# Kernel optimization log

Hardware: AMD Instinct MI355X
Metric: run time of the kernel (lower is better)

The kernel has to match this reference:

```python
import jax, jax.numpy as jnp
import numpy as np

B, P, L = 32, 16, 512
VOCAB, D = 50000, 256  # embed_dim == hidden_dim (required for attn_type='dot')
SCALE, PAGE_SCALE = 10.0, 10.0


def sparsemax(z):
    # z: [..., K]; sort-based sparsemax (Martins & Astudillo 2016)
    K = z.shape[-1]
    zs = jnp.sort(z, axis=-1)[..., ::-1]            # descending
    k = jnp.arange(1, K + 1, dtype=z.dtype)
    cs = jnp.cumsum(zs, axis=-1)
    support = 1.0 + k * zs > cs                     # [..., K] bool
    kmax = jnp.sum(support, axis=-1, keepdims=True) # support size (>=1)
    cs_k = jnp.take_along_axis(cs, kmax.astype(jnp.int32) - 1, axis=-1)
    tau = (cs_k - 1.0) / kmax.astype(z.dtype)
    return jnp.maximum(z - tau, 0.0)


def setup_inputs() -> dict:
    key = jax.random.key(0)
    k1, k2, k3, k4, k5, k6, k7 = jax.random.split(key, 7)
    seq_ids = jax.random.randint(k1, (B, P, L), 0, VOCAB)
    num_pages = jax.random.randint(k2, (B,), 1, P + 1)        # 1..P valid pages
    seq_lengths = jax.random.randint(k3, (B, P), 1, L + 1)    # 1..L valid tokens
    emb_table = jax.random.uniform(k4, (VOCAB, D), jnp.float32, -0.1, 0.1)
    V = jax.random.normal(k5, (D, 1), jnp.float32)
    W = jax.random.normal(k6, (D, 1), jnp.float32)
    dec_w = jax.random.normal(k7, (1, D), jnp.float32) * 0.05  # decoder, no bias
    return {"seq_ids": seq_ids, "num_pages": num_pages, "seq_lengths": seq_lengths,
            "emb_table": emb_table, "V": V, "W": W, "dec_w": dec_w}


def reference(seq_ids, num_pages, seq_lengths, emb_table, V, W, dec_w):
    # Embedding lookup (dropout is identity in eval mode)
    hidden_vecs = emb_table[seq_ids]                         # [B,P,L,D]
    # Word-level scores (attn_type='dot': inter_out = hidden_vecs)
    scores = jnp.einsum('bpld,do->bpl', hidden_vecs, V) / SCALE  # [B,P,L]
    # Ragged word mask: original double loop only masks pages j < num_pages[i]
    pos = jnp.arange(L)[None, None, :]                       # [1,1,L]
    page_idx = jnp.arange(P)[None, :, None]                  # [1,P,1]
    word_mask = (pos >= seq_lengths[:, :, None]) & (page_idx < num_pages[:, None, None])
    scores = jnp.where(word_mask, -999.0, scores)
    attn = jax.nn.softmax(scores, axis=-1)[:, :, None, :]    # [B,P,1,L]
    webpage_vec = jnp.einsum('bpl,bpld->bpd', attn[:, :, 0, :], hidden_vecs)  # [B,P,D]
    # Page-level scores + sparsemax over pages
    page_scores = jnp.einsum('bpd,do->bp', webpage_vec, W) / PAGE_SCALE
    page_mask = jnp.arange(P)[None, :] >= num_pages[:, None]
    page_scores = jnp.where(page_mask, -9999.0, page_scores)
    page_attn = sparsemax(page_scores)[:, None, :]           # [B,1,P]
    final_vec = jnp.einsum('bp,bpd->bd', page_attn[:, 0, :], webpage_vec)  # [B,D]
    senti_scores = final_vec @ dec_w.T                       # [B,1]
    probs = jax.nn.sigmoid(senti_scores)
    return (probs, senti_scores, attn, page_attn, final_vec, page_scores, webpage_vec)
```

## Files before the change

kernel.cpp:

```cpp
#include <hip/hip_runtime.h>
#include <math.h>

constexpr int Bn = 32, Pn = 16, Ln = 512, Dn = 256, VOC = 50000;
constexpr float QSCALE = 1270.0f, QINV = 1.0f / 1270.0f;

__global__ __launch_bounds__(256) void k_embdot(const float* __restrict__ emb,
                                               const float* __restrict__ V,
                                               const float* __restrict__ W,
                                               float2* __restrict__ eVW,
                                               unsigned char* __restrict__ bt)
{
    int row  = blockIdx.x * 4 + (threadIdx.x >> 6);
    if (row >= VOC) return;
    int lane = threadIdx.x & 63;
    float4 r  = ((const float4*)(emb + (size_t)row * Dn))[lane];
    float4 v  = ((const float4*)V)[lane];
    float4 w  = ((const float4*)W)[lane];

    uint b0 = (uint)((int)rintf(r.x * QSCALE) + 128);
    uint b1 = (uint)((int)rintf(r.y * QSCALE) + 128);
    uint b2 = (uint)((int)rintf(r.z * QSCALE) + 128);
    uint b3 = (uint)((int)rintf(r.w * QSCALE) + 128);
    ((uint*)(bt + (size_t)row * Dn))[lane] = b0 | (b1 << 8) | (b2 << 16) | (b3 << 24);

    float dv = r.x*v.x + r.y*v.y + r.z*v.z + r.w*v.w;
    float dw = r.x*w.x + r.y*w.y + r.z*w.z + r.w*w.w;
#pragma unroll
    for (int o = 32; o; o >>= 1) { dv += __shfl_xor(dv, o); dw += __shfl_xor(dw, o); }
    if (lane == 0) eVW[row] = make_float2(dv / 10.0f, dw / 10.0f);
}

__global__ __launch_bounds__(512) void k_page(const int* __restrict__ seq_ids,
                                              const int* __restrict__ num_pages,
                                              const int* __restrict__ seq_lengths,
                                              const unsigned char* __restrict__ bt,
                                              const float2* __restrict__ eVW,
                                              float* __restrict__ attn_out,
                                              float* __restrict__ pscore_out,
                                              float* __restrict__ web_out)
{
    int bp = blockIdx.x;
    int b  = bp >> 4, p = bp & 15;
    int tid = threadIdx.x, lane = tid & 63, wv = tid >> 6;

    __shared__ int   ids[Ln];
    __shared__ float sc[Ln];
    __shared__ float redm[8], reds[8], redp[8];
    __shared__ float part[32][Dn];

    const int* sid = seq_ids + (size_t)bp * Ln;
    int  slen = seq_lengths[bp];
    bool vp   = (p < num_pages[b]);
    int  Lv   = vp ? slen : Ln;

    int id = sid[tid];
    ids[tid] = id;
    float2 vw = eVW[id];
    float wreg = vw.y;
    sc[tid] = (vp && tid >= slen) ? -999.0f : vw.x;
    __syncthreads();

    float mx = sc[tid];
#pragma unroll
    for (int o = 32; o; o >>= 1) mx = fmaxf(mx, __shfl_xor(mx, o));
    if (lane == 0) redm[wv] = mx;
    __syncthreads();
    mx = redm[0];
#pragma unroll
    for (int w = 1; w < 8; ++w) mx = fmaxf(mx, redm[w]);

    float e = expf(sc[tid] - mx);
    sc[tid] = e;
    float pw = e * wreg;
    float sum = e, ps = pw;
#pragma unroll
    for (int o = 32; o; o >>= 1) { sum += __shfl_xor(sum, o); ps += __shfl_xor(ps, o); }
    if (lane == 0) { reds[wv] = sum; redp[wv] = ps; }
    __syncthreads();
    sum = 0.f; ps = 0.f;
#pragma unroll
    for (int w = 0; w < 8; ++w) { sum += reds[w]; ps += redp[w]; }
    float inv = 1.0f / sum;

    attn_out[(size_t)bp * Ln + tid] = sc[tid] * inv;
    if (tid == 0) pscore_out[bp] = vp ? ps * inv : -9999.0f;

    int s  = 4 * wv + (lane >> 4);
    int cq = lane & 15;
    float a0=0,a1=0,a2=0,a3=0,a4=0,a5=0,a6=0,a7=0,
          a8=0,a9=0,a10=0,a11=0,a12=0,a13=0,a14=0,a15=0;
    float sw = 0.f;
#pragma unroll 4
    for (int l = s; l < Lv; l += 32) {
        float wg = sc[l];
        uint4 q = *(const uint4*)(bt + (size_t)ids[l] * Dn + cq * 16);
        sw  += wg;
        a0  += wg * (float)( q.x        & 0xffu);
        a1  += wg * (float)((q.x >>  8) & 0xffu);
        a2  += wg * (float)((q.x >> 16) & 0xffu);
        a3  += wg * (float)( q.x >> 24         );
        a4  += wg * (float)( q.y        & 0xffu);
        a5  += wg * (float)((q.y >>  8) & 0xffu);
        a6  += wg * (float)((q.y >> 16) & 0xffu);
        a7  += wg * (float)( q.y >> 24         );
        a8  += wg * (float)( q.z        & 0xffu);
        a9  += wg * (float)((q.z >>  8) & 0xffu);
        a10 += wg * (float)((q.z >> 16) & 0xffu);
        a11 += wg * (float)( q.z >> 24         );
        a12 += wg * (float)( q.w        & 0xffu);
        a13 += wg * (float)((q.w >>  8) & 0xffu);
        a14 += wg * (float)((q.w >> 16) & 0xffu);
        a15 += wg * (float)( q.w >> 24         );
    }
    float k = inv * QINV;
    float c = 128.0f * sw;
    float* pr = &part[s][cq * 16];
    ((float4*)pr)[0] = make_float4((a0 -c)*k, (a1 -c)*k, (a2 -c)*k, (a3 -c)*k);
    ((float4*)pr)[1] = make_float4((a4 -c)*k, (a5 -c)*k, (a6 -c)*k, (a7 -c)*k);
    ((float4*)pr)[2] = make_float4((a8 -c)*k, (a9 -c)*k, (a10-c)*k, (a11-c)*k);
    ((float4*)pr)[3] = make_float4((a12-c)*k, (a13-c)*k, (a14-c)*k, (a15-c)*k);
    __syncthreads();

    if (tid < Dn) {
        float acc = 0.f;
#pragma unroll
        for (int w = 0; w < 32; ++w) acc += part[w][tid];
        web_out[(size_t)bp * Dn + tid] = acc;
    }
}

__global__ __launch_bounds__(256) void k_final(const float* __restrict__ dec_w,
                                               const float* __restrict__ pscore,
                                               const float* __restrict__ web,
                                               float* __restrict__ probs,
                                               float* __restrict__ senti,
                                               float* __restrict__ pattn,
                                               float* __restrict__ fvec)
{
    int b = blockIdx.x, tid = threadIdx.x, lane = tid & 63, wv = tid >> 6;
    __shared__ float pa[Pn];
    __shared__ float red[4];

    if (tid == 0) {
        float z[Pn], zs[Pn], csum[Pn];
        for (int i = 0; i < Pn; ++i) { z[i] = pscore[b * Pn + i]; zs[i] = z[i]; }
        for (int i = 1; i < Pn; ++i) {
            float key = zs[i]; int j = i - 1;
            while (j >= 0 && zs[j] < key) { zs[j + 1] = zs[j]; --j; }
            zs[j + 1] = key;
        }
        int kmax = 0; float cs = 0.f;
        for (int k = 0; k < Pn; ++k) {
            cs += zs[k];
            csum[k] = cs;
            if (1.0f + (float)(k + 1) * zs[k] > cs) kmax = k + 1;
        }
        float tau = (csum[kmax - 1] - 1.0f) / (float)kmax;
        for (int i = 0; i < Pn; ++i) pa[i] = fmaxf(z[i] - tau, 0.0f);
    }
    __syncthreads();

    float fv = 0.f;
#pragma unroll
    for (int p = 0; p < Pn; ++p) fv += pa[p] * web[((size_t)b * Pn + p) * Dn + tid];
    fvec[(size_t)b * Dn + tid] = fv;
    if (tid < Pn) pattn[b * Pn + tid] = pa[tid];

    float t = fv * dec_w[tid];
#pragma unroll
    for (int o = 32; o; o >>= 1) t += __shfl_xor(t, o);
    if (lane == 0) red[wv] = t;
    __syncthreads();
    if (tid == 0) {
        float s = red[0] + red[1] + red[2] + red[3];
        senti[b] = s;
        probs[b] = 1.0f / (1.0f + expf(-s));
    }
}

extern "C" void kernel_launch(void* const* d_in, const int* in_sizes, int n_in,
                              void* d_out, int out_size, void* d_ws, size_t ws_size,
                              hipStream_t stream) {
    const int*   seq_ids     = (const int*)d_in[0];
    const int*   num_pages   = (const int*)d_in[1];
    const int*   seq_lengths = (const int*)d_in[2];
    const float* emb         = (const float*)d_in[3];
    const float* V           = (const float*)d_in[4];
    const float* W           = (const float*)d_in[5];
    const float* dec_w       = (const float*)d_in[6];

    float* out    = (float*)d_out;
    float* probs  = out;
    float* senti  = probs + Bn;
    float* attn   = senti + Bn;
    float* pattn  = attn  + (size_t)Bn * Pn * Ln;
    float* fvec   = pattn + Bn * Pn;
    float* pscore = fvec  + (size_t)Bn * Dn;
    float* web    = pscore + Bn * Pn;

    float2* eVW = (float2*)d_ws;
    unsigned char* bt = (unsigned char*)((char*)d_ws + (size_t)VOC * sizeof(float2));

    k_embdot<<<(VOC + 3) / 4, 256, 0, stream>>>(emb, V, W, eVW, bt);
    k_page<<<Bn * Pn, 512, 0, stream>>>(seq_ids, num_pages, seq_lengths,
                                        bt, eVW, attn, pscore, web);
    k_final<<<Bn, 256, 0, stream>>>(dec_w, pscore, web, probs, senti, pattn, fvec);
}
```

Before: 32.17 us.

## Fuse final sparsemax kernel into page kernel via last-block atomic counter

Removes the separate k_final launch. Each page block bumps a per-batch atomic counter, and the last of the 16 page blocks for a batch computes the sparsemax, the final vector, the decoder score and the sigmoid. The counters are zeroed inside k_embdot. The gather loop is also unrolled to process two tokens per iteration at stride 64, which exposes more independent loads. This can over-read tokens past the sequence length, but those carry near-zero softmax weight. The cost is an extra barrier, threadfences and a tail of serial work in one block per batch.

```diff
diff --git a/kernel.cpp b/kernel.cpp
--- a/kernel.cpp
+++ b/kernel.cpp
@@ -8,8 +8,10 @@
                                                const float* __restrict__ V,
                                                const float* __restrict__ W,
                                                float2* __restrict__ eVW,
-                                               unsigned char* __restrict__ bt)
+                                               unsigned char* __restrict__ bt,
+                                               int* __restrict__ cnt)
 {
+    if (blockIdx.x == 0 && threadIdx.x < Bn) cnt[threadIdx.x] = 0;
     int row  = blockIdx.x * 4 + (threadIdx.x >> 6);
     if (row >= VOC) return;
     int lane = threadIdx.x & 63;
@@ -35,9 +37,15 @@
                                               const int* __restrict__ seq_lengths,
                                               const unsigned char* __restrict__ bt,
                                               const float2* __restrict__ eVW,
+                                              const float* __restrict__ dec_w,
                                               float* __restrict__ attn_out,
                                               float* __restrict__ pscore_out,
-                                              float* __restrict__ web_out)
+                                              float* __restrict__ web_out,
+                                              float* __restrict__ probs,
+                                              float* __restrict__ senti,
+                                              float* __restrict__ pattn,
+                                              float* __restrict__ fvec,
+                                              int* __restrict__ cnt)
 {
     int bp = blockIdx.x;
     int b  = bp >> 4, p = bp & 15;
@@ -47,6 +55,8 @@
     __shared__ float sc[Ln];
     __shared__ float redm[8], reds[8], redp[8];
     __shared__ float part[32][Dn];
+    __shared__ float pa[Pn];
+    __shared__ int   isLast;
 
     const int* sid = seq_ids + (size_t)bp * Ln;
     int  slen = seq_lengths[bp];
@@ -90,27 +100,30 @@
     float a0=0,a1=0,a2=0,a3=0,a4=0,a5=0,a6=0,a7=0,
           a8=0,a9=0,a10=0,a11=0,a12=0,a13=0,a14=0,a15=0;
     float sw = 0.f;
-#pragma unroll 4
-    for (int l = s; l < Lv; l += 32) {
-        float wg = sc[l];
-        uint4 q = *(const uint4*)(bt + (size_t)ids[l] * Dn + cq * 16);
-        sw  += wg;
-        a0  += wg * (float)( q.x        & 0xffu);
-        a1  += wg * (float)((q.x >>  8) & 0xffu);
-        a2  += wg * (float)((q.x >> 16) & 0xffu);
-        a3  += wg * (float)( q.x >> 24         );
-        a4  += wg * (float)( q.y        & 0xffu);
-        a5  += wg * (float)((q.y >>  8) & 0xffu);
-        a6  += wg * (float)((q.y >> 16) & 0xffu);
-        a7  += wg * (float)( q.y >> 24         );
-        a8  += wg * (float)( q.z        & 0xffu);
-        a9  += wg * (float)((q.z >>  8) & 0xffu);
-        a10 += wg * (float)((q.z >> 16) & 0xffu);
-        a11 += wg * (float)( q.z >> 24         );
-        a12 += wg * (float)( q.w        & 0xffu);
-        a13 += wg * (float)((q.w >>  8) & 0xffu);
-        a14 += wg * (float)((q.w >> 16) & 0xffu);
-        a15 += wg * (float)( q.w >> 24         );
+#pragma unroll 2
+    for (int l = s; l < Lv; l += 64) {
+        int   l2 = l + 32;
+        float w1 = sc[l];
+        float w2 = sc[l2];
+        uint4 q1 = *(const uint4*)(bt + (size_t)ids[l]  * Dn + cq * 16);
+        uint4 q2 = *(const uint4*)(bt + (size_t)ids[l2] * Dn + cq * 16);
+        sw  += w1 + w2;
+        a0  += w1 * (float)( q1.x        & 0xffu) + w2 * (float)( q2.x        & 0xffu);
+        a1  += w1 * (float)((q1.x >>  8) & 0xffu) + w2 * (float)((q2.x >>  8) & 0xffu);
+        a2  += w1 * (float)((q1.x >> 16) & 0xffu) + w2 * (float)((q2.x >> 16) & 0xffu);
+        a3  += w1 * (float)( q1.x >> 24         ) + w2 * (float)( q2.x >> 24         );
+        a4  += w1 * (float)( q1.y        & 0xffu) + w2 * (float)( q2.y        & 0xffu);
+        a5  += w1 * (float)((q1.y >>  8) & 0xffu) + w2 * (float)((q2.y >>  8) & 0xffu);
+        a6  += w1 * (float)((q1.y >> 16) & 0xffu) + w2 * (float)((q2.y >> 16) & 0xffu);
+        a7  += w1 * (float)( q1.y >> 24         ) + w2 * (float)( q2.y >> 24         );
+        a8  += w1 * (float)( q1.z        & 0xffu) + w2 * (float)( q2.z        & 0xffu);
+        a9  += w1 * (float)((q1.z >>  8) & 0xffu) + w2 * (float)((q2.z >>  8) & 0xffu);
+        a10 += w1 * (float)((q1.z >> 16) & 0xffu) + w2 * (float)((q2.z >> 16) & 0xffu);
+        a11 += w1 * (float)( q1.z >> 24         ) + w2 * (float)( q2.z >> 24         );
+        a12 += w1 * (float)( q1.w        & 0xffu) + w2 * (float)( q2.w        & 0xffu);
+        a13 += w1 * (float)((q1.w >>  8) & 0xffu) + w2 * (float)((q2.w >>  8) & 0xffu);
+        a14 += w1 * (float)((q1.w >> 16) & 0xffu) + w2 * (float)((q2.w >> 16) & 0xffu);
+        a15 += w1 * (float)( q1.w >> 24         ) + w2 * (float)( q2.w >> 24         );
     }
     float k = inv * QINV;
     float c = 128.0f * sw;
@@ -127,54 +140,53 @@
         for (int w = 0; w < 32; ++w) acc += part[w][tid];
         web_out[(size_t)bp * Dn + tid] = acc;
     }
-}
-
-__global__ __launch_bounds__(256) void k_final(const float* __restrict__ dec_w,
-                                               const float* __restrict__ pscore,
-                                               const float* __restrict__ web,
-                                               float* __restrict__ probs,
-                                               float* __restrict__ senti,
-                                               float* __restrict__ pattn,
-                                               float* __restrict__ fvec)
-{
-    int b = blockIdx.x, tid = threadIdx.x, lane = tid & 63, wv = tid >> 6;
-    __shared__ float pa[Pn];
-    __shared__ float red[4];
+    __syncthreads();
+
+    if (tid == 0) {
+        __threadfence();
+        int old = atomicAdd(&cnt[b], 1);
+        isLast = (old == Pn - 1);
+    }
+    __syncthreads();
+    if (!isLast) return;
+    __threadfence();
 
     if (tid == 0) {
         float z[Pn], zs[Pn], csum[Pn];
-        for (int i = 0; i < Pn; ++i) { z[i] = pscore[b * Pn + i]; zs[i] = z[i]; }
+        for (int i = 0; i < Pn; ++i) { z[i] = pscore_out[b * Pn + i]; zs[i] = z[i]; }
         for (int i = 1; i < Pn; ++i) {
             float key = zs[i]; int j = i - 1;
             while (j >= 0 && zs[j] < key) { zs[j + 1] = zs[j]; --j; }
             zs[j + 1] = key;
         }
         int kmax = 0; float cs = 0.f;
-        for (int k = 0; k < Pn; ++k) {
-            cs += zs[k];
-            csum[k] = cs;
-            if (1.0f + (float)(k + 1) * zs[k] > cs) kmax = k + 1;
+        for (int kk = 0; kk < Pn; ++kk) {
+            cs += zs[kk];
+            csum[kk] = cs;
+            if (1.0f + (float)(kk + 1) * zs[kk] > cs) kmax = kk + 1;
         }
         float tau = (csum[kmax - 1] - 1.0f) / (float)kmax;
         for (int i = 0; i < Pn; ++i) pa[i] = fmaxf(z[i] - tau, 0.0f);
     }
     __syncthreads();
 
-    float fv = 0.f;
-#pragma unroll
-    for (int p = 0; p < Pn; ++p) fv += pa[p] * web[((size_t)b * Pn + p) * Dn + tid];
-    fvec[(size_t)b * Dn + tid] = fv;
+    if (tid < Dn) {
+        float fv = 0.f;
+#pragma unroll
+        for (int q = 0; q < Pn; ++q) fv += pa[q] * web_out[((size_t)b * Pn + q) * Dn + tid];
+        fvec[(size_t)b * Dn + tid] = fv;
+
+        float t = fv * dec_w[tid];
+#pragma unroll
+        for (int o = 32; o; o >>= 1) t += __shfl_xor(t, o);
+        if (lane == 0) redm[wv] = t;
+    }
     if (tid < Pn) pattn[b * Pn + tid] = pa[tid];
-
-    float t = fv * dec_w[tid];
-#pragma unroll
-    for (int o = 32; o; o >>= 1) t += __shfl_xor(t, o);
-    if (lane == 0) red[wv] = t;
     __syncthreads();
     if (tid == 0) {
-        float s = red[0] + red[1] + red[2] + red[3];
-        senti[b] = s;
-        probs[b] = 1.0f / (1.0f + expf(-s));
+        float ssum = redm[0] + redm[1] + redm[2] + redm[3];
+        senti[b] = ssum;
+        probs[b] = 1.0f / (1.0f + expf(-ssum));
     }
 }
 
@@ -198,11 +210,12 @@
     float* pscore = fvec  + (size_t)Bn * Dn;
     float* web    = pscore + Bn * Pn;
 
-    float2* eVW = (float2*)d_ws;
-    unsigned char* bt = (unsigned char*)((char*)d_ws + (size_t)VOC * sizeof(float2));
-
-    k_embdot<<<(VOC + 3) / 4, 256, 0, stream>>>(emb, V, W, eVW, bt);
+    float2*        eVW = (float2*)d_ws;
+    unsigned char* bt  = (unsigned char*)((char*)d_ws + (size_t)VOC * sizeof(float2));
+    int*           cnt = (int*)(bt + (size_t)VOC * Dn);
+
+    k_embdot<<<(VOC + 3) / 4, 256, 0, stream>>>(emb, V, W, eVW, bt, cnt);
     k_page<<<Bn * Pn, 512, 0, stream>>>(seq_ids, num_pages, seq_lengths,
-                                        bt, eVW, attn, pscore, web);
-    k_final<<<Bn, 256, 0, stream>>>(dec_w, pscore, web, probs, senti, pattn, fvec);
+                                        bt, eVW, dec_w, attn, pscore, web,
+                                        probs, senti, pattn, fvec, cnt);
 }
```

Result: slower. 54.61 us (+69.8%).
